# Optimization experiments

Measured on AMD Instinct MI355X. Metric: run time of the kernel, lower is better.

Reference implementation:

```python
import jax, jax.numpy as jnp
import numpy as np

B, D = 16384, 2048          # batch, input_dim
N_TOP, N_CLASS = 8, 16      # top labels, bottom labels per top (uniform, contiguous ids)

def setup_inputs() -> dict:
    key = jax.random.key(0)
    k1, k2, k3, k4, k5 = jax.random.split(key, 5)
    INIT = 0.2  # matches init_weight uniform(-0.2, 0.2)
    return {
        "features": jax.random.normal(k1, (B, D), dtype=jnp.float32),
        "top_W": jax.random.uniform(k2, (N_TOP, D), minval=-INIT, maxval=INIT, dtype=jnp.float32),
        "top_b": jax.random.uniform(k3, (N_TOP,), minval=-INIT, maxval=INIT, dtype=jnp.float32),
        "bottom_W": jax.random.uniform(k4, (N_TOP, D, N_CLASS), minval=-INIT, maxval=INIT, dtype=jnp.float32),
        "bottom_b": jax.random.uniform(k5, (N_TOP, N_CLASS), minval=-INIT, maxval=INIT, dtype=jnp.float32),
    }

def reference(features, top_W, top_b, bottom_W, bottom_b):
    # dropout p=0.0 -> identity
    # top gate: linear + sigmoid, (b, n_top)
    top_scores = jax.nn.sigmoid(features @ top_W.T + top_b)
    # all per-top-label expert linears as one batched GEMM: (b, n_top, n_class)
    bottom_logits = jnp.einsum('bd,tdc->btc', features, bottom_W) + bottom_b
    bottom_scores = jax.nn.softmax(bottom_logits, axis=-1)
    # scatter-combine: bottom ids of top i are contiguous [i*N_CLASS, (i+1)*N_CLASS),
    # so the column scatter is a reshape. (b, n_bottom_labels)
    final_scores = (top_scores[:, :, None] * bottom_scores).reshape(features.shape[0], N_TOP * N_CLASS)
    return final_scores
```

## Files before the change

### kernel.cpp

```cpp
#include <hip/hip_runtime.h>


#define D_DIM 2048
#define NTILE 9
#define M_ROWS 64
#define KC 64
#define NCHUNK (D_DIM / KC)

using f32x4  = float __attribute__((ext_vector_type(4)));
using half8  = _Float16 __attribute__((ext_vector_type(8)));
using fp16x2 = __fp16 __attribute__((ext_vector_type(2)));

typedef const void __attribute__((address_space(1)))* gas_ptr;
typedef void __attribute__((address_space(3)))* lds_ptr;

static __device__ __forceinline__ void dma16(const void* g, void* l) {
    __builtin_amdgcn_global_load_lds((gas_ptr)g, (lds_ptr)l, 16, 0, 0);
}

__global__ void prep_weights(const float* __restrict__ topW,
                             const float* __restrict__ botW,
                             _Float16* __restrict__ S) {
    int idx = blockIdx.x * blockDim.x + threadIdx.x;
    if (idx >= 64 * NTILE * 64) return;
    int lane = idx & 63;
    int tmp  = idx >> 6;
    int nt   = tmp % NTILE;
    int kc   = tmp / NTILE;
    int n     = nt * 16 + (lane & 15);
    int kbase = kc * 32 + (lane >> 4) * 8;

    _Float16 v[8];
    #pragma unroll
    for (int j = 0; j < 8; j++) {
        int k = kbase + j;
        float x = 0.0f;
        if (n < 8) {
            x = topW[n * D_DIM + k];
        } else if (n < 136) {
            int t = (n - 8) >> 4, c = (n - 8) & 15;
            x = botW[(t * D_DIM + k) * 16 + c];
        }
        v[j] = (_Float16)x;
    }
    *(half8*)(S + (size_t)idx * 8) = *(half8*)v;
}

static __device__ __forceinline__ half8 pack_af(f32x4 a, f32x4 b) {
    fp16x2 p0 = __builtin_amdgcn_cvt_pkrtz(a[0], a[1]);
    fp16x2 p1 = __builtin_amdgcn_cvt_pkrtz(a[2], a[3]);
    fp16x2 p2 = __builtin_amdgcn_cvt_pkrtz(b[0], b[1]);
    fp16x2 p3 = __builtin_amdgcn_cvt_pkrtz(b[2], b[3]);
    half8 r;
    r[0] = (_Float16)p0[0]; r[1] = (_Float16)p0[1];
    r[2] = (_Float16)p1[0]; r[3] = (_Float16)p1[1];
    r[4] = (_Float16)p2[0]; r[5] = (_Float16)p2[1];
    r[6] = (_Float16)p3[0]; r[7] = (_Float16)p3[1];
    return r;
}

__global__ __launch_bounds__(256, 1) void hc_fused(
        const float* __restrict__ feat, const _Float16* __restrict__ Bsw,
        const float* __restrict__ top_b, const float* __restrict__ bot_b,
        float* __restrict__ out) {
    __shared__ float    Abuf[2][4096];
    __shared__ _Float16 Bbuf[2][9216];
    __shared__ float    red[4][16][148];

    const int tid  = threadIdx.x;
    const int lane = tid & 63, wave = tid >> 6;
    const int quad = lane >> 4, low = lane & 15;
    const int brow0 = blockIdx.x * M_ROWS;

    const float*    aSrc = feat + (size_t)(brow0 + lane) * D_DIM;
    const _Float16* bSrc = Bsw + (size_t)lane * 8;

    f32x4 acc[NTILE];
    #pragma unroll
    for (int i = 0; i < NTILE; i++) acc[i] = (f32x4)0.0f;

    #pragma unroll
    for (int i = wave; i < 16; i += 4)
        dma16(aSrc + i * 4, &Abuf[0][i * 256]);
    #pragma unroll
    for (int j = wave; j < 18; j += 4)
        dma16(bSrc + j * 512, &Bbuf[0][j * 512]);

    for (int c = 0; c < NCHUNK; c++) {
        __syncthreads();
        if (c + 1 < NCHUNK) {
            const int nb = (c + 1) & 1;
            const float*    an = aSrc + (c + 1) * KC;
            const _Float16* bn = bSrc + (size_t)(c + 1) * 18 * 512;
            #pragma unroll
            for (int i = wave; i < 16; i += 4)
                dma16(an + i * 4, &Abuf[nb][i * 256]);
            #pragma unroll
            for (int j = wave; j < 18; j += 4)
                dma16(bn + j * 512, &Bbuf[nb][j * 512]);
        }
        const int cb = c & 1;
        #pragma unroll
        for (int s = 0; s < 2; s++) {
            const int kq = s * 8 + quad * 2;
            f32x4 a0 = *(const f32x4*)&Abuf[cb][(kq * 64 + wave * 16 + low) * 4];
            f32x4 a1 = *(const f32x4*)&Abuf[cb][((kq + 1) * 64 + wave * 16 + low) * 4];
            const half8 af = pack_af(a0, a1);
            #pragma unroll
            for (int nt = 0; nt < NTILE; nt++) {
                half8 bf = *(const half8*)&Bbuf[cb][(s * NTILE + nt) * 512 + lane * 8];
                acc[nt] = __builtin_amdgcn_mfma_f32_16x16x32_f16(af, bf, acc[nt], 0, 0, 0);
            }
        }
    }

    #pragma unroll
    for (int nt = 0; nt < NTILE; nt++) {
        #pragma unroll
        for (int r = 0; r < 4; r++) {
            red[wave][quad * 4 + r][nt * 16 + low] = acc[nt][r];
        }
    }
    __syncthreads();

    #pragma unroll
    for (int rr = 0; rr < 2; rr++) {
        const int row = rr * 32 + (tid >> 3);
        const int top = tid & 7;
        const int wv = row >> 4, r = row & 15;

        float zt = top_b[top] + red[wv][r][top];
        const float sig = 1.0f / (1.0f + __expf(-zt));

        float z[16];
        float zmax = -1e30f;
        #pragma unroll
        for (int c = 0; c < 16; c++) {
            float v = bot_b[top * 16 + c] + red[wv][r][8 + top * 16 + c];
            z[c] = v;
            zmax = fmaxf(zmax, v);
        }
        float s = 0.0f;
        #pragma unroll
        for (int c = 0; c < 16; c++) { z[c] = __expf(z[c] - zmax); s += z[c]; }
        const float scale = sig / s;

        float* o = out + (size_t)(brow0 + row) * 128 + top * 16;
        #pragma unroll
        for (int c = 0; c < 16; c += 4) {
            f32x4 v = { z[c] * scale, z[c+1] * scale, z[c+2] * scale, z[c+3] * scale };
            *(f32x4*)(o + c) = v;
        }
    }
}

extern "C" void kernel_launch(void* const* d_in, const int* in_sizes, int n_in,
                              void* d_out, int out_size, void* d_ws, size_t ws_size,
                              hipStream_t stream) {
    const float* feat  = (const float*)d_in[0];
    const float* topW  = (const float*)d_in[1];
    const float* topB  = (const float*)d_in[2];
    const float* botW  = (const float*)d_in[3];
    const float* botB  = (const float*)d_in[4];
    float* out = (float*)d_out;
    _Float16* Bsw = (_Float16*)d_ws;

    prep_weights<<<(64 * NTILE * 64 + 255) / 256, 256, 0, stream>>>(topW, botW, Bsw);
    hc_fused<<<16384 / M_ROWS, 256, 0, stream>>>(feat, Bsw, topB, botB, out);
}
```

Measured before the change: 220.6 us.

## Halve rows per block to 32 with two waves and row-major A tile layout

Cuts each block from 64 rows and 4 waves to 32 rows and 2 waves, doubling the grid to 512 blocks so more blocks are spread across the CUs. The A tile moves from a k-major interleaved layout to a row-major 32x64 layout, with each lane DMAing contiguous 16-byte segments of a row and the MFMA operand read as two consecutive float4s. The fp16 weight chunk is still loaded in full by every block, so total weight traffic per output row doubles, and the row-major LDS reads may cause bank conflicts.

```diff
diff --git a/kernel.cpp b/kernel.cpp
--- a/kernel.cpp
+++ b/kernel.cpp
@@ -3,7 +3,7 @@
 
 #define D_DIM 2048
 #define NTILE 9
-#define M_ROWS 64
+#define M_ROWS 32
 #define KC 64
 #define NCHUNK (D_DIM / KC)
 
@@ -59,52 +59,52 @@
     return r;
 }
 
-__global__ __launch_bounds__(256, 1) void hc_fused(
+__global__ __launch_bounds__(128, 1) void hc_fused(
         const float* __restrict__ feat, const _Float16* __restrict__ Bsw,
         const float* __restrict__ top_b, const float* __restrict__ bot_b,
         float* __restrict__ out) {
-    __shared__ float    Abuf[2][4096];
-    __shared__ _Float16 Bbuf[2][9216];
-    __shared__ float    red[4][16][148];
+    __shared__ float    Abuf[2][M_ROWS * KC];
+    __shared__ _Float16 Bbuf[2][18 * 512];
+    __shared__ float    red[M_ROWS][148];
 
     const int tid  = threadIdx.x;
     const int lane = tid & 63, wave = tid >> 6;
     const int quad = lane >> 4, low = lane & 15;
     const int brow0 = blockIdx.x * M_ROWS;
 
-    const float*    aSrc = feat + (size_t)(brow0 + lane) * D_DIM;
-    const _Float16* bSrc = Bsw + (size_t)lane * 8;
+    const float* aLane = feat + (size_t)(brow0 + (lane >> 4)) * D_DIM + (lane & 15) * 4;
+    const _Float16* bLane = Bsw + lane * 8;
 
     f32x4 acc[NTILE];
     #pragma unroll
     for (int i = 0; i < NTILE; i++) acc[i] = (f32x4)0.0f;
 
     #pragma unroll
-    for (int i = wave; i < 16; i += 4)
-        dma16(aSrc + i * 4, &Abuf[0][i * 256]);
+    for (int i = wave; i < 8; i += 2)
+        dma16(aLane + i * 4 * D_DIM, &Abuf[0][i * 256 + lane * 4]);
     #pragma unroll
-    for (int j = wave; j < 18; j += 4)
-        dma16(bSrc + j * 512, &Bbuf[0][j * 512]);
+    for (int j = wave; j < 18; j += 2)
+        dma16(bLane + j * 512, &Bbuf[0][j * 512 + lane * 8]);
 
     for (int c = 0; c < NCHUNK; c++) {
         __syncthreads();
         if (c + 1 < NCHUNK) {
             const int nb = (c + 1) & 1;
-            const float*    an = aSrc + (c + 1) * KC;
-            const _Float16* bn = bSrc + (size_t)(c + 1) * 18 * 512;
+            const float*    an = aLane + (c + 1) * KC;
+            const _Float16* bn = bLane + (size_t)(c + 1) * 18 * 512;
             #pragma unroll
-            for (int i = wave; i < 16; i += 4)
-                dma16(an + i * 4, &Abuf[nb][i * 256]);
+            for (int i = wave; i < 8; i += 2)
+                dma16(an + i * 4 * D_DIM, &Abuf[nb][i * 256 + lane * 4]);
             #pragma unroll
-            for (int j = wave; j < 18; j += 4)
-                dma16(bn + j * 512, &Bbuf[nb][j * 512]);
+            for (int j = wave; j < 18; j += 2)
+                dma16(bn + j * 512, &Bbuf[nb][j * 512 + lane * 8]);
         }
         const int cb = c & 1;
         #pragma unroll
         for (int s = 0; s < 2; s++) {
-            const int kq = s * 8 + quad * 2;
-            f32x4 a0 = *(const f32x4*)&Abuf[cb][(kq * 64 + wave * 16 + low) * 4];
-            f32x4 a1 = *(const f32x4*)&Abuf[cb][((kq + 1) * 64 + wave * 16 + low) * 4];
+            const float* ar = &Abuf[cb][(wave * 16 + low) * KC + s * 32 + quad * 8];
+            f32x4 a0 = *(const f32x4*)(ar);
+            f32x4 a1 = *(const f32x4*)(ar + 4);
             const half8 af = pack_af(a0, a1);
             #pragma unroll
             for (int nt = 0; nt < NTILE; nt++) {
@@ -118,25 +118,24 @@
     for (int nt = 0; nt < NTILE; nt++) {
         #pragma unroll
         for (int r = 0; r < 4; r++) {
-            red[wave][quad * 4 + r][nt * 16 + low] = acc[nt][r];
+            red[wave * 16 + quad * 4 + r][nt * 16 + low] = acc[nt][r];
         }
     }
     __syncthreads();
 
     #pragma unroll
     for (int rr = 0; rr < 2; rr++) {
-        const int row = rr * 32 + (tid >> 3);
+        const int row = rr * 16 + (tid >> 3);
         const int top = tid & 7;
-        const int wv = row >> 4, r = row & 15;
 
-        float zt = top_b[top] + red[wv][r][top];
+        float zt = top_b[top] + red[row][top];
         const float sig = 1.0f / (1.0f + __expf(-zt));
 
         float z[16];
         float zmax = -1e30f;
         #pragma unroll
         for (int c = 0; c < 16; c++) {
-            float v = bot_b[top * 16 + c] + red[wv][r][8 + top * 16 + c];
+            float v = bot_b[top * 16 + c] + red[row][8 + top * 16 + c];
             z[c] = v;
             zmax = fmaxf(zmax, v);
         }
@@ -166,5 +165,5 @@
     _Float16* Bsw = (_Float16*)d_ws;
 
     prep_weights<<<(64 * NTILE * 64 + 255) / 256, 256, 0, stream>>>(topW, botW, Bsw);
-    hc_fused<<<16384 / M_ROWS, 256, 0, stream>>>(feat, Bsw, topB, botB, out);
+    hc_fused<<<16384 / M_ROWS, 128, 0, stream>>>(feat, Bsw, topB, botB, out);
 }
```

New measurement: 220.6 us. No clear change (-0.0%).
